# Kernel optimization log

Measured on AMD Instinct MI355X. Metric: run time of the kernel, lower is better.

## Reference

```python
import jax, jax.numpy as jnp
import numpy as np

LOG_2PI = 1.8378770664093453  # log(2*pi)

B, N_FEAT = 4096, 1024
R, K, D = 64, 32, 16  # n_regions, n_batch (distributions per region), region size


def setup_inputs() -> dict:
    key = jax.random.key(0)
    k1, k2, k3, k4 = jax.random.split(key, 4)
    x = jax.random.normal(k1, (B, N_FEAT), dtype=jnp.float32)
    # Regions: partition-like index sets over the feature space (equal size D).
    regions = jax.random.randint(k2, (R, D), 0, N_FEAT, dtype=jnp.int64)
    # Per-region diag-Gaussian params (means ~ N(0, 0.1), scales near 1.0).
    means = 0.1 * jax.random.normal(k3, (R, K, D), dtype=jnp.float32)
    scales = 0.9 + 0.2 * jax.random.uniform(k4, (R, K, D), dtype=jnp.float32)
    return {"x": x, "regions": regions, "means": means, "scales": scales}


def reference(x, regions, means, scales):
    # Gather per-region features in one shot: [B, R, D]
    xg = x[:, regions]
    # Diag-Gaussian log-prob, broadcast over the K distributions per region.
    # z: [B, R, K, D]
    z = (xg[:, :, None, :] - means[None]) / scales[None]
    log_det = jnp.sum(jnp.log(scales), axis=-1)  # [R, K]
    ll = -0.5 * jnp.sum(z * z, axis=-1) - log_det[None] - 0.5 * D * LOG_2PI
    return ll  # [B, R, K] == stack over regions of MVNDiag.log_prob
```

## Files before the change

### kernel.cpp

```cpp
#include <hip/hip_runtime.h>

typedef __attribute__((ext_vector_type(8))) short short8;
typedef __attribute__((ext_vector_type(4))) float floatx4;

#define NB 4096
#define NF 1024
#define NR 64
#define NK 32
#define ND 16
#define HALF_D_LOG2PI 14.702988531274762f

__device__ __forceinline__ unsigned f2bf_bits(float f) {
    unsigned u = __float_as_uint(f);
    return (u + 0x7fffu + ((u >> 16) & 1u)) >> 16;
}

__global__ __launch_bounds__(256) void prep_kernel(
    const float* __restrict__ means, const float* __restrict__ scales,
    unsigned short* __restrict__ wfrag, float* __restrict__ cv)
{
    __shared__ float Asm[NK][ND];
    __shared__ float Bsm[NK][ND];
    __shared__ float csum[NK][8];
    const int r = blockIdx.x;
    const int t = threadIdx.x;

    {
        int k  = t >> 3;
        int d0 = (t & 7) * 2;
        const float* m = means  + ((size_t)r * NK + k) * ND + d0;
        const float* s = scales + ((size_t)r * NK + k) * ND + d0;
        float partial = 0.f;
#pragma unroll
        for (int q = 0; q < 2; ++q) {
            float sd = s[q], md = m[q];
            float a  = 1.f / sd;
            float a2 = a * a;
            Asm[k][d0 + q] = -0.5f * a2;
            Bsm[k][d0 + q] = md * a2;
            float c = md * a;
            partial += -0.5f * c * c - logf(sd);
        }
        csum[k][t & 7] = partial;
    }
    __syncthreads();
    if (t < NK) {
        float acc = 0.f;
#pragma unroll
        for (int q = 0; q < 8; ++q) acc += csum[t][q];
        cv[r * NK + t] = acc - HALF_D_LOG2PI;
    }

    if (t < 128) {
        const int nt   = t >> 6;
        const int lane = t & 63;
        const int n    = lane & 15;
        const int qd   = lane >> 4;
        const int kk   = nt * 16 + n;
        unsigned px[4];
#pragma unroll
        for (int j2 = 0; j2 < 4; ++j2) {
            int K0 = qd * 8 + j2 * 2;
            int K1 = K0 + 1;
            float v0 = (K0 < 16) ? Asm[kk][K0] : Bsm[kk][K0 - 16];
            float v1 = (K1 < 16) ? Asm[kk][K1] : Bsm[kk][K1 - 16];
            px[j2] = f2bf_bits(v0) | (f2bf_bits(v1) << 16);
        }
        *(uint4*)(wfrag + (((size_t)r * 2 + nt) * 64 + lane) * 8) = *(uint4*)px;
    }
}

__global__ __launch_bounds__(512, 4) void fused_kernel(
    const float* __restrict__ x, const int* __restrict__ regions,
    const unsigned short* __restrict__ wfrag, const float* __restrict__ cv,
    float* __restrict__ out)
{
    __shared__ __align__(16) char lds[81920];
    float*    xs   = (float*)lds;
    int*      ridx = (int*)(lds + 16 * 1028 * 4);
    unsigned* xgd  = (unsigned*)lds;

    const int t  = threadIdx.x;
    const int bt = blockIdx.x;
    const int b0 = bt * 16;

#pragma unroll
    for (int j = t; j < NR * ND; j += 512) {
        int rr = j >> 4, d = j & 15;
        ridx[rr * 17 + d] = regions[j];
    }
    {
        const float4* src = (const float4*)(x + (size_t)b0 * NF);
#pragma unroll
        for (int i = 0; i < 8; ++i) {
            int j = t + i * 512;
            int row = j >> 8, c4 = j & 255;
            *(float4*)(xs + row * 1028 + c4 * 4) = src[row * 256 + c4];
        }
    }
    __syncthreads();

    const int rl = t >> 3;
    const int bb = t & 7;
    int idxv[ND];
#pragma unroll
    for (int d = 0; d < ND; ++d) idxv[d] = ridx[rl * 17 + d];

    unsigned pk[2][16];
#pragma unroll
    for (int pp = 0; pp < 2; ++pp) {
        const int b = bb + pp * 8;
#pragma unroll
        for (int d = 0; d < ND; d += 2) {
            float x0 = xs[b * 1028 + idxv[d]];
            float x1 = xs[b * 1028 + idxv[d + 1]];
            pk[pp][d >> 1]       = f2bf_bits(x0 * x0) | (f2bf_bits(x1 * x1) << 16);
            pk[pp][8 + (d >> 1)] = f2bf_bits(x0)      | (f2bf_bits(x1)      << 16);
        }
    }
    __syncthreads();

    {
        const int s = rl & 3;
#pragma unroll
        for (int pp = 0; pp < 2; ++pp) {
            int row = rl * 16 + bb + pp * 8;
            unsigned* wp = xgd + row * 20;
#pragma unroll
            for (int c = 0; c < 4; ++c)
                *(uint4*)(wp + ((c ^ s) << 2)) = ((uint4*)pk[pp])[c];
        }
    }
    __syncthreads();

    const int wv   = t >> 6;
    const int L    = t & 63;
    const int col  = L & 15;
    const int quad = L >> 4;
    const short* wfs = (const short*)wfrag;

#pragma unroll 2
    for (int i = 0; i < 8; ++i) {
        int r   = wv * 8 + i;
        int row = r * 16 + col;
        int s   = r & 3;
        const unsigned* rp = xgd + row * 20;
        uint4 ca = *(const uint4*)(rp + ((quad ^ s) << 2));
        short8 a = *(short8*)&ca;

        size_t wb = (size_t)r * 2 * 512 + (size_t)L * 8;
        short8 w0 = *(const short8*)(wfs + wb);
        short8 w1 = *(const short8*)(wfs + wb + 512);

        floatx4 z = {0.f, 0.f, 0.f, 0.f};
        floatx4 acc0 = __builtin_amdgcn_mfma_f32_16x16x32_bf16(a, w0, z, 0, 0, 0);
        floatx4 acc1 = __builtin_amdgcn_mfma_f32_16x16x32_bf16(a, w1, z, 0, 0, 0);

        float c0 = cv[r * NK + col];
        float c1 = cv[r * NK + 16 + col];
        int brow = bt * 16 + quad * 4;
#pragma unroll
        for (int g = 0; g < 4; ++g) {
            size_t ob = (size_t)(brow + g) * (NR * NK) + (size_t)r * NK;
            out[ob + col]      = acc0[g] + c0;
            out[ob + 16 + col] = acc1[g] + c1;
        }
    }
}

extern "C" void kernel_launch(void* const* d_in, const int* in_sizes, int n_in,
                              void* d_out, int out_size, void* d_ws, size_t ws_size,
                              hipStream_t stream) {
    const float* x       = (const float*)d_in[0];
    const int*   regions = (const int*)d_in[1];
    const float* means   = (const float*)d_in[2];
    const float* scales  = (const float*)d_in[3];
    float* out = (float*)d_out;

    char* ws = (char*)d_ws;
    unsigned short* wfrag = (unsigned short*)ws;
    float*          cvp   = (float*)(ws + 131072);

    prep_kernel<<<dim3(NR), 256, 0, stream>>>(means, scales, wfrag, cvp);
    fused_kernel<<<dim3(NB / 16), 512, 0, stream>>>(x, regions, wfrag, cvp, out);
}
```

Baseline: 83.99 us.

## Split regions across two blocks and gather MFMA operands directly from LDS

Each fused-kernel block now handles only half of the regions, with 256 threads and twice as many blocks. Each lane gathers its own A-fragment values straight from the staged x tile, squaring them when in the upper-half operand, which removes the intermediate packed buffer and two barriers. Region indices and per-distribution constants are now staged in LDS. The cost is that every x tile is loaded twice from global memory (once per region half), and the LDS gathers are scattered and may hit bank conflicts.

```diff
diff --git a/kernel.cpp b/kernel.cpp
--- a/kernel.cpp
+++ b/kernel.cpp
@@ -70,85 +70,65 @@
     }
 }
 
-__global__ __launch_bounds__(512, 4) void fused_kernel(
+__global__ __launch_bounds__(256, 2) void fused_kernel(
     const float* __restrict__ x, const int* __restrict__ regions,
     const unsigned short* __restrict__ wfrag, const float* __restrict__ cv,
     float* __restrict__ out)
 {
-    __shared__ __align__(16) char lds[81920];
-    float*    xs   = (float*)lds;
-    int*      ridx = (int*)(lds + 16 * 1028 * 4);
-    unsigned* xgd  = (unsigned*)lds;
+    __shared__ __align__(16) float xs[16][1028];
+    __shared__ __align__(16) int   ridx[32][16];
+    __shared__ __align__(16) float cvs[32][32];
 
     const int t  = threadIdx.x;
-    const int bt = blockIdx.x;
+    const int bt = blockIdx.x >> 1;
+    const int rh = blockIdx.x & 1;
     const int b0 = bt * 16;
+    const int r0 = rh * 32;
 
-#pragma unroll
-    for (int j = t; j < NR * ND; j += 512) {
-        int rr = j >> 4, d = j & 15;
-        ridx[rr * 17 + d] = regions[j];
-    }
     {
         const float4* src = (const float4*)(x + (size_t)b0 * NF);
 #pragma unroll
-        for (int i = 0; i < 8; ++i) {
-            int j = t + i * 512;
+        for (int i = 0; i < 16; ++i) {
+            int j = t + i * 256;
             int row = j >> 8, c4 = j & 255;
-            *(float4*)(xs + row * 1028 + c4 * 4) = src[row * 256 + c4];
+            *(float4*)(&xs[row][c4 * 4]) = src[row * 256 + c4];
         }
     }
-    __syncthreads();
-
-    const int rl = t >> 3;
-    const int bb = t & 7;
-    int idxv[ND];
-#pragma unroll
-    for (int d = 0; d < ND; ++d) idxv[d] = ridx[rl * 17 + d];
-
-    unsigned pk[2][16];
-#pragma unroll
-    for (int pp = 0; pp < 2; ++pp) {
-        const int b = bb + pp * 8;
-#pragma unroll
-        for (int d = 0; d < ND; d += 2) {
-            float x0 = xs[b * 1028 + idxv[d]];
-            float x1 = xs[b * 1028 + idxv[d + 1]];
-            pk[pp][d >> 1]       = f2bf_bits(x0 * x0) | (f2bf_bits(x1 * x1) << 16);
-            pk[pp][8 + (d >> 1)] = f2bf_bits(x0)      | (f2bf_bits(x1)      << 16);
-        }
-    }
-    __syncthreads();
-
-    {
-        const int s = rl & 3;
-#pragma unroll
-        for (int pp = 0; pp < 2; ++pp) {
-            int row = rl * 16 + bb + pp * 8;
-            unsigned* wp = xgd + row * 20;
-#pragma unroll
-            for (int c = 0; c < 4; ++c)
-                *(uint4*)(wp + ((c ^ s) << 2)) = ((uint4*)pk[pp])[c];
-        }
-    }
+    if (t < 128)
+        ((int4*)ridx)[t] = ((const int4*)(regions + r0 * ND))[t];
+    ((float4*)cvs)[t] = ((const float4*)(cv + r0 * NK))[t];
     __syncthreads();
 
     const int wv   = t >> 6;
     const int L    = t & 63;
     const int col  = L & 15;
     const int quad = L >> 4;
+    const bool sq  = quad < 2;
+    const int dsl  = (quad & 1) * 8;
+    const float* xc = &xs[col][0];
     const short* wfs = (const short*)wfrag;
 
 #pragma unroll 2
     for (int i = 0; i < 8; ++i) {
-        int r   = wv * 8 + i;
-        int row = r * 16 + col;
-        int s   = r & 3;
-        const unsigned* rp = xgd + row * 20;
-        uint4 ca = *(const uint4*)(rp + ((quad ^ s) << 2));
-        short8 a = *(short8*)&ca;
+        const int r  = wv * 8 + i;
+        const int rg = r0 + r;
 
-        size_t wb = (size_t)r * 2 * 512 + (size_t)L * 8;
+        int4 i4a = *(const int4*)&ridx[r][dsl];
+        int4 i4b = *(const int4*)&ridx[r][dsl + 4];
+        float v0 = xc[i4a.x], v1 = xc[i4a.y], v2 = xc[i4a.z], v3 = xc[i4a.w];
+        float v4 = xc[i4b.x], v5 = xc[i4b.y], v6 = xc[i4b.z], v7 = xc[i4b.w];
+        if (sq) {
+            v0 *= v0; v1 *= v1; v2 *= v2; v3 *= v3;
+            v4 *= v4; v5 *= v5; v6 *= v6; v7 *= v7;
+        }
+        unsigned p[4];
+        p[0] = f2bf_bits(v0) | (f2bf_bits(v1) << 16);
+        p[1] = f2bf_bits(v2) | (f2bf_bits(v3) << 16);
+        p[2] = f2bf_bits(v4) | (f2bf_bits(v5) << 16);
+        p[3] = f2bf_bits(v6) | (f2bf_bits(v7) << 16);
+        short8 a = *(short8*)p;
+
+        size_t wb = (size_t)rg * 2 * 512 + (size_t)L * 8;
         short8 w0 = *(const short8*)(wfs + wb);
         short8 w1 = *(const short8*)(wfs + wb + 512);
 
@@ -156,12 +136,12 @@
         floatx4 acc0 = __builtin_amdgcn_mfma_f32_16x16x32_bf16(a, w0, z, 0, 0, 0);
         floatx4 acc1 = __builtin_amdgcn_mfma_f32_16x16x32_bf16(a, w1, z, 0, 0, 0);
 
-        float c0 = cv[r * NK + col];
-        float c1 = cv[r * NK + 16 + col];
-        int brow = bt * 16 + quad * 4;
+        float c0 = cvs[r][col];
+        float c1 = cvs[r][16 + col];
+        int brow = b0 + quad * 4;
 #pragma unroll
         for (int g = 0; g < 4; ++g) {
-            size_t ob = (size_t)(brow + g) * (NR * NK) + (size_t)r * NK;
+            size_t ob = (size_t)(brow + g) * (NR * NK) + (size_t)rg * NK;
             out[ob + col]      = acc0[g] + c0;
             out[ob + 16 + col] = acc1[g] + c1;
         }
@@ -182,5 +162,5 @@
     float*          cvp   = (float*)(ws + 131072);
 
     prep_kernel<<<dim3(NR), 256, 0, stream>>>(means, scales, wfrag, cvp);
-    fused_kernel<<<dim3(NB / 16), 512, 0, stream>>>(x, regions, wfrag, cvp, out);
+    fused_kernel<<<dim3((NB / 16) * 2), 256, 0, stream>>>(x, regions, wfrag, cvp, out);
 }
```

After: 84.82 us. Within noise of the previous version (+1.0%).
